# Optimization experiments

Hardware: AMD Instinct MI355X
Metric: run time of the kernel (lower is better)

The kernel has to match this reference:

```python
import jax, jax.numpy as jnp
import numpy as np

GAMMA = 20.0
GAMMA2 = 10.0
KATZ_FACTOR = 0.5
EPS = 1e-8


def setup_inputs() -> dict:
    key = jax.random.key(0)
    k1, k2, k3, k4 = jax.random.split(key, 4)
    b, n_way, k_shot, q, c, h, w = 16, 5, 5, 75, 640, 5, 5
    return {
        "support_xf": jax.random.normal(k1, (b, n_way * k_shot, c, h, w), jnp.float32),
        "support_y": jax.random.randint(k2, (b, n_way * k_shot), 0, n_way),
        "query_xf": jax.random.normal(k3, (b, q, c, h, w), jnp.float32),
        "query_y": jax.random.randint(k4, (b, q), 0, n_way),
        "n_way": n_way,
        "k_shot": k_shot,
    }


def _mel_loss(support_xf, query_xf, query_y, n_way, k_shot):
    b, s, c, h, w = support_xf.shape
    q = query_xf.shape[1]
    hw = h * w
    # averaging-based similarities: mean over shots, cosine over channel dim
    sup = support_xf.reshape(b, n_way, k_shot, c, hw).mean(2)          # (b, n_way, c, hw)
    sup = sup / (jnp.linalg.norm(sup, axis=2, keepdims=True) + EPS)
    qry = query_xf.reshape(b, q, c, hw)                                 # (b, q, c, hw)
    qry = qry / (jnp.linalg.norm(qry, axis=2, keepdims=True) + EPS)
    # S[b,q,way,i,j] = cos(query pixel i, support pixel j)
    S = jnp.einsum('bqci,bwcj->bqwij', qry, sup)                        # (b, q, n_way, hw, hw)
    M_q = hw
    M_s = n_way * hw
    S = S.transpose(0, 1, 3, 2, 4).reshape(b * q, M_q, M_s)             # (N, M_q, M_s)
    N = b * q

    # gamma-scaled softmax transition matrices
    T_sq = jax.nn.softmax(GAMMA * S, axis=-1)                           # (N, M_q, M_s)
    T_qs = jax.nn.softmax(GAMMA2 * jnp.swapaxes(S, -1, -2), axis=-1)    # (N, M_s, M_q)

    # bipartite block transition matrix T (N, M_s+M_q, M_s+M_q)
    top = jnp.concatenate([jnp.zeros((N, M_s, M_s), S.dtype),
                           jnp.swapaxes(T_sq, -1, -2)], axis=-1)
    bot = jnp.concatenate([jnp.swapaxes(T_qs, -1, -2),
                           jnp.zeros((N, M_q, M_q), S.dtype)], axis=-1)
    T = jnp.concatenate([top, bot], axis=-2)

    # katz = (inv(I - a*T) - I) @ 1  ==  solve(I - a*T, 1) - 1
    A = jnp.eye(M_s + M_q, dtype=S.dtype) - KATZ_FACTOR * T
    ones = jnp.ones((N, M_s + M_q, 1), S.dtype)
    katz = jnp.linalg.solve(A, ones)[..., 0] - 1.0                      # (N, M_s+M_q)

    pk = katz[:, :M_s]
    pk = pk / pk.sum(-1, keepdims=True)
    predicts = pk.reshape(N, n_way, -1).sum(-1)                         # (N, n_way)

    yv = query_y.reshape(N)
    logp = jnp.log(predicts)
    loss = -jnp.mean(logp[jnp.arange(N), yv])                           # NLLLoss
    return loss


def reference(support_xf, support_y, query_xf, query_y, n_way, k_shot):
    return _mel_loss(support_xf, query_xf, query_y, n_way, k_shot)
```

## Files before the change

### kernel.cpp

```cpp
#include <hip/hip_runtime.h>
#include <math.h>

#define NN   1200
#define EPSF 1e-8f

typedef _Float16 h8 __attribute__((ext_vector_type(8)));
typedef __attribute__((ext_vector_type(16))) float f16v;

#define AHI 0
#define ALO 16384
#define BHI 32768
#define BLO 49152

__global__ __launch_bounds__(256) void kA1(const float* __restrict__ sxf,
                                           float* __restrict__ supmean) {
  const int blk = blockIdx.x;
  const int b = blk / 25, rem = blk % 25, w = rem / 5, ck = rem % 5;
  const int c0 = ck * 128;
  const int tid = threadIdx.x;
  __shared__ float lds[3200];
  const float* base = sxf + (size_t)(b * 25 + w * 5) * 16000 + (size_t)c0 * 25;

  for (int f0 = tid * 4; f0 < 3200; f0 += 1024) {
    float4 a  = *(const float4*)(base + f0);
    float4 b1 = *(const float4*)(base + 16000 + f0);
    float4 c1 = *(const float4*)(base + 32000 + f0);
    float4 d1 = *(const float4*)(base + 48000 + f0);
    float4 e1 = *(const float4*)(base + 64000 + f0);
    lds[f0 + 0] = (a.x + b1.x + c1.x + d1.x + e1.x) * 0.2f;
    lds[f0 + 1] = (a.y + b1.y + c1.y + d1.y + e1.y) * 0.2f;
    lds[f0 + 2] = (a.z + b1.z + c1.z + d1.z + e1.z) * 0.2f;
    lds[f0 + 3] = (a.w + b1.w + c1.w + d1.w + e1.w) * 0.2f;
  }
  __syncthreads();
  for (int g = tid; g < 3200; g += 256) {
    int j = g >> 7, cc = g & 127;
    supmean[(size_t)(b * 125 + w * 25 + j) * 640 + c0 + cc] = lds[cc * 25 + j];
  }
}

__global__ __launch_bounds__(256) void kA2(const float* __restrict__ supmean,
                                           ushort* __restrict__ sup) {
  const int r = blockIdx.x * 4 + (threadIdx.x >> 6);
  const int lane = threadIdx.x & 63;
  const int b = r / 125, s = r % 125;
  const float* row = supmean + (size_t)r * 640;
  float4 v0 = *(const float4*)(row + lane * 4);
  float4 v1 = *(const float4*)(row + 256 + lane * 4);
  float4 v2 = {0.f, 0.f, 0.f, 0.f};
  if (lane < 32) v2 = *(const float4*)(row + 512 + lane * 4);
  float ssq = v0.x*v0.x + v0.y*v0.y + v0.z*v0.z + v0.w*v0.w
            + v1.x*v1.x + v1.y*v1.y + v1.z*v1.z + v1.w*v1.w
            + v2.x*v2.x + v2.y*v2.y + v2.z*v2.z + v2.w*v2.w;
#pragma unroll
  for (int d = 32; d; d >>= 1) ssq += __shfl_xor(ssq, d);
  const float rinv = 1.f / (sqrtf(ssq) + EPSF);
  ushort* dst = sup + (size_t)b * 160000 + (size_t)s * 640;
#pragma unroll
  for (int seg = 0; seg < 3; ++seg) {
    if (seg == 2 && lane >= 32) break;
    float4 v = (seg == 0) ? v0 : ((seg == 1) ? v1 : v2);
    int c = seg * 256 + lane * 4;
    float vv[4] = { v.x * rinv, v.y * rinv, v.z * rinv, v.w * rinv };
    ushort hh[4], ll[4];
#pragma unroll
    for (int u = 0; u < 4; ++u) {
      _Float16 h = (_Float16)vv[u];
      float rr = vv[u] - (float)h;
      _Float16 l = (_Float16)rr;
      hh[u] = __builtin_bit_cast(ushort, h);
      ll[u] = __builtin_bit_cast(ushort, l);
    }
    uint2 ph = { (uint)hh[0] | ((uint)hh[1] << 16), (uint)hh[2] | ((uint)hh[3] << 16) };
    uint2 pl = { (uint)ll[0] | ((uint)ll[1] << 16), (uint)ll[2] | ((uint)ll[3] << 16) };
    *(uint2*)(dst + c) = ph;
    *(uint2*)(dst + 80000 + c) = pl;
  }
}

__device__ __forceinline__ void load_chunk(const float* __restrict__ qbase5,
                                           const ushort* __restrict__ supb,
                                           int k0, int tid,
                                           float (&aq)[8][4], uint4 (&bq)[8]) {
#pragma unroll
  for (int j = 0; j < 8; ++j) {
    int t = tid + j * 256;
    if (t < 2000) {
      int q = t / 400, rem = t % 400, c4 = rem / 25, i = rem % 25;
      const float* qp = qbase5 + (size_t)q * 16000 + (size_t)(k0 + c4 * 4) * 25 + i;
      aq[j][0] = qp[0]; aq[j][1] = qp[25]; aq[j][2] = qp[50]; aq[j][3] = qp[75];
    }
  }
#pragma unroll
  for (int j = 0; j < 8; ++j) {
    int t = tid + j * 256;
    if (t < 2000) {
      int hl = (t >= 1000) ? 1 : 0;
      int r2 = t - hl * 1000;
      int row = r2 >> 3, seg = r2 & 7;
      bq[j] = *(const uint4*)(supb + (size_t)hl * 80000 + (size_t)row * 640 + k0 + seg * 8);
    }
  }
}

__device__ __forceinline__ void store_chunk(char* st, int tid,
                                            float (&aq)[8][4], uint4 (&bq)[8],
                                            float (&pn)[8]) {
#pragma unroll
  for (int j = 0; j < 8; ++j) {
    int t = tid + j * 256;
    if (t < 2000) {
      int q = t / 400, rem = t % 400, c4 = rem / 25, i = rem % 25;
      int row = q * 25 + i;
      ushort hh[4], ll[4];
      float ss = 0.f;
#pragma unroll
      for (int u = 0; u < 4; ++u) {
        float v = aq[j][u];
        ss = fmaf(v, v, ss);
        _Float16 h = (_Float16)v;
        float rr = v - (float)h;
        _Float16 l = (_Float16)rr;
        hh[u] = __builtin_bit_cast(ushort, h);
        ll[u] = __builtin_bit_cast(ushort, l);
      }
      pn[j] += ss;
      uint2 ph = { (uint)hh[0] | ((uint)hh[1] << 16), (uint)hh[2] | ((uint)hh[3] << 16) };
      uint2 pl = { (uint)ll[0] | ((uint)ll[1] << 16), (uint)ll[2] | ((uint)ll[3] << 16) };
      int off = (row * 128 + c4 * 8) ^ ((row & 7) << 4);
      *(uint2*)(st + AHI + off) = ph;
      *(uint2*)(st + ALO + off) = pl;
    }
  }
#pragma unroll
  for (int j = 0; j < 8; ++j) {
    int t = tid + j * 256;
    if (t < 2000) {
      int hl = (t >= 1000) ? 1 : 0;
      int r2 = t - hl * 1000;
      int row = r2 >> 3, seg = r2 & 7;
      int off = (row * 128 + seg * 16) ^ ((row & 7) << 4);
      *(uint4*)(st + BHI + hl * 16384 + off) = bq[j];
    }
  }
}

__global__ __launch_bounds__(256, 1) void kG(const float* __restrict__ qxf,
                                             const ushort* __restrict__ sup,
                                             float* __restrict__ Sg) {
  const int blk = blockIdx.x;
  const int b = blk / 15, qg = blk % 15;
  const int tid = threadIdx.x;
  const int lane = tid & 63, l31 = lane & 31, hi32 = lane >> 5;
  const int wv = tid >> 6, wr = wv >> 1, wc = wv & 1;
  __shared__ __align__(16) char st[65536];
  __shared__ float nsq[128], rinv_s[128];

  const float* qbase5 = qxf + (size_t)(b * 75 + qg * 5) * 16000;
  const ushort* supb = sup + (size_t)b * 160000;

  if (tid < 96) {
    int r = 125 + tid / 32, cb = (tid % 32) * 4;
    int off = (r * 128 + cb) ^ ((r & 7) << 4);
    *(uint*)(st + AHI + off) = 0u; *(uint*)(st + ALO + off) = 0u;
    *(uint*)(st + BHI + off) = 0u; *(uint*)(st + BLO + off) = 0u;
  }
  if (tid < 128) nsq[tid] = 0.f;

  f16v acc[2][2];
#pragma unroll
  for (int rt = 0; rt < 2; ++rt)
#pragma unroll
    for (int ct = 0; ct < 2; ++ct)
#pragma unroll
      for (int r = 0; r < 16; ++r) acc[rt][ct][r] = 0.f;

  float aA[8][4], aB[8][4];
  uint4 bA[8], bB[8];
  float pn[8];
#pragma unroll
  for (int j = 0; j < 8; ++j) pn[j] = 0.f;

  load_chunk(qbase5, supb, 0, tid, aA, bA);

#define MFMA_PHASE()                                                          \
  {                                                                           \
    _Pragma("unroll")                                                         \
    for (int ks = 0; ks < 4; ++ks) {                                          \
      const int kb = ks * 32 + hi32 * 16;                                     \
      h8 ahf[2], alf[2], bhf[2], blf[2];                                      \
      _Pragma("unroll")                                                       \
      for (int rt = 0; rt < 2; ++rt) {                                        \
        int ar = wr * 64 + rt * 32 + l31;                                     \
        int off = (ar * 128 + kb) ^ ((ar & 7) << 4);                          \
        ahf[rt] = *(const h8*)(st + AHI + off);                               \
        alf[rt] = *(const h8*)(st + ALO + off);                               \
      }                                                                       \
      _Pragma("unroll")                                                       \
      for (int ct = 0; ct < 2; ++ct) {                                        \
        int br = wc * 64 + ct * 32 + l31;                                     \
        int off = (br * 128 + kb) ^ ((br & 7) << 4);                          \
        bhf[ct] = *(const h8*)(st + BHI + off);                               \
        blf[ct] = *(const h8*)(st + BLO + off);                               \
      }                                                                       \
      _Pragma("unroll")                                                       \
      for (int rt = 0; rt < 2; ++rt)                                          \
        _Pragma("unroll")                                                     \
        for (int ct = 0; ct < 2; ++ct) {                                      \
          acc[rt][ct] = __builtin_amdgcn_mfma_f32_32x32x16_f16(ahf[rt], bhf[ct], acc[rt][ct], 0, 0, 0); \
          acc[rt][ct] = __builtin_amdgcn_mfma_f32_32x32x16_f16(alf[rt], bhf[ct], acc[rt][ct], 0, 0, 0); \
          acc[rt][ct] = __builtin_amdgcn_mfma_f32_32x32x16_f16(ahf[rt], blf[ct], acc[rt][ct], 0, 0, 0); \
        }                                                                     \
    }                                                                         \
  }

  for (int ch = 0; ch < 10; ch += 2) {
    __syncthreads();
    store_chunk(st, tid, aA, bA, pn);
    if (ch + 1 < 10) load_chunk(qbase5, supb, (ch + 1) * 64, tid, aB, bB);
    __syncthreads();
    MFMA_PHASE();
    __syncthreads();
    store_chunk(st, tid, aB, bB, pn);
    if (ch + 2 < 10) load_chunk(qbase5, supb, (ch + 2) * 64, tid, aA, bA);
    __syncthreads();
    MFMA_PHASE();
  }

#pragma unroll
  for (int j = 0; j < 8; ++j) {
    int t = tid + j * 256;
    if (t < 2000) {
      int q = t / 400, rem = t % 400, i = rem % 25;
      atomicAdd(&nsq[q * 25 + i], pn[j]);
    }
  }
  __syncthreads();
  if (tid < 125) rinv_s[tid] = 1.f / (sqrtf(nsq[tid]) + EPSF);
  __syncthreads();

#pragma unroll
  for (int rt = 0; rt < 2; ++rt) {
#pragma unroll
    for (int r = 0; r < 16; ++r) {
      int rowg = wr * 64 + rt * 32 + (r & 3) + 8 * (r >> 2) + 4 * hi32;
      if (rowg < 125) {
        float rv = rinv_s[rowg];
        int n = b * 75 + qg * 5 + rowg / 25;
        int i = rowg % 25;
#pragma unroll
        for (int ct = 0; ct < 2; ++ct) {
          int col = wc * 64 + ct * 32 + l31;
          Sg[(size_t)n * 3200 + i * 128 + col] = acc[rt][ct][r] * rv;
        }
      }
    }
  }
}

#define LD 132
__global__ __launch_bounds__(256) void kT(const float* __restrict__ Sg,
                                          const int* __restrict__ qy,
                                          float* __restrict__ out) {
  const int n = blockIdx.x;
  const int tid = threadIdx.x;
  __shared__ __align__(16) float S[25 * LD];
  __shared__ __align__(16) float TqsT[25 * LD];
  __shared__ float Bm[625], rhs[25], xv[25], Pk[5];

  const float* sgn = Sg + (size_t)n * 3200;
  for (int idx = tid; idx < 800; idx += 256) {
    int row = idx >> 5, q4 = idx & 31;
    *(float4*)(S + row * LD + q4 * 4) = *(const float4*)(sgn + row * 128 + q4 * 4);
  }
  if (tid < 5) Pk[tid] = 0.f;
  if (tid >= 32 && tid < 57) {
    int i = tid - 32;
    TqsT[i * LD + 125] = 0.f; TqsT[i * LD + 126] = 0.f; TqsT[i * LD + 127] = 0.f;
  }
  __syncthreads();

  if (tid < 125) {
    float mx = -1e30f;
#pragma unroll
    for (int i = 0; i < 25; ++i) mx = fmaxf(mx, S[i * LD + tid]);
    float sm = 0.f;
#pragma unroll
    for (int i = 0; i < 25; ++i) {
      float e = __expf(10.f * (S[i * LD + tid] - mx));
      TqsT[i * LD + tid] = e; sm += e;
    }
    float rs = 1.f / sm;
#pragma unroll
    for (int i = 0; i < 25; ++i) TqsT[i * LD + tid] *= rs;
  }
  __syncthreads();
  if (tid < 200) {
    int i = tid >> 3, l = tid & 7;
    float* Srow = S + i * LD;
    float mx = -1e30f;
    for (int ss = l; ss < 125; ss += 8) mx = fmaxf(mx, Srow[ss]);
    mx = fmaxf(mx, __shfl_xor(mx, 1, 8));
    mx = fmaxf(mx, __shfl_xor(mx, 2, 8));
    mx = fmaxf(mx, __shfl_xor(mx, 4, 8));
    float sm = 0.f;
    for (int ss = l; ss < 128; ss += 8) {
      float e = 0.f;
      if (ss < 125) { e = __expf(20.f * (Srow[ss] - mx)); sm += e; }
      Srow[ss] = e;
    }
    sm += __shfl_xor(sm, 1, 8);
    sm += __shfl_xor(sm, 2, 8);
    sm += __shfl_xor(sm, 4, 8);
    float rs = 1.f / sm;
    for (int ss = l; ss < 125; ss += 8) Srow[ss] *= rs;
  }
  __syncthreads();

  for (int ii = tid; ii < 625; ii += 256) {
    int i = ii / 25, ip = ii % 25;
    const float* ta = TqsT + i * LD;
    const float* tb = S + ip * LD;
    float4 s4 = { 0.f, 0.f, 0.f, 0.f };
#pragma unroll
    for (int q4 = 0; q4 < 32; ++q4) {
      float4 a4 = *(const float4*)(ta + q4 * 4);
      float4 b4 = *(const float4*)(tb + q4 * 4);
      s4.x = fmaf(a4.x, b4.x, s4.x); s4.y = fmaf(a4.y, b4.y, s4.y);
      s4.z = fmaf(a4.z, b4.z, s4.z); s4.w = fmaf(a4.w, b4.w, s4.w);
    }
    Bm[ii] = (s4.x + s4.y) + (s4.z + s4.w);
  }
  if (tid < 25) {
    const float* ta = TqsT + tid * LD;
    float4 s4 = { 0.f, 0.f, 0.f, 0.f };
#pragma unroll
    for (int q4 = 0; q4 < 32; ++q4) {
      float4 a4 = *(const float4*)(ta + q4 * 4);
      s4.x += a4.x; s4.y += a4.y; s4.z += a4.z; s4.w += a4.w;
    }
    rhs[tid] = 1.f + 0.5f * ((s4.x + s4.y) + (s4.z + s4.w));
  }
  __syncthreads();

  if (tid < 64) {
    float Brow[25], x, rh;
    if (tid < 25) {
      rh = rhs[tid]; x = rh;
#pragma unroll
      for (int ip = 0; ip < 25; ++ip) Brow[ip] = Bm[tid * 25 + ip];
    } else {
      rh = 0.f; x = 0.f;
#pragma unroll
      for (int ip = 0; ip < 25; ++ip) Brow[ip] = 0.f;
    }
#pragma unroll
    for (int it = 0; it < 16; ++it) {
      float sum = 0.f;
#pragma unroll
      for (int ip = 0; ip < 25; ++ip) sum = fmaf(Brow[ip], __shfl(x, ip), sum);
      x = rh + 0.25f * sum;
    }
    if (tid < 25) xv[tid] = x;
  }
  __syncthreads();

  if (tid < 125) {
    float kz = 0.f;
#pragma unroll
    for (int i = 0; i < 25; ++i) kz = fmaf(S[i * LD + tid], xv[i], kz);
    atomicAdd(&Pk[tid / 25], kz);
  }
  __syncthreads();
  if (tid == 0) {
    float den = Pk[0] + Pk[1] + Pk[2] + Pk[3] + Pk[4];
    int y = qy[n];
    float v = -(logf(Pk[y]) - logf(den)) * (1.0f / (float)NN);
    atomicAdd(out, v);
  }
}

extern "C" void kernel_launch(void* const* d_in, const int* in_sizes, int n_in,
                              void* d_out, int out_size, void* d_ws, size_t ws_size,
                              hipStream_t stream) {
  const float* sxf = (const float*)d_in[0];
  const float* qxf = (const float*)d_in[2];
  const int*   qy  = (const int*)d_in[3];
  float* out = (float*)d_out;
  float*  supmean = (float*)d_ws;
  ushort* sup     = (ushort*)((char*)d_ws + 5120000);
  float*  Sgw     = (float*)((char*)d_ws + 10240000);

  hipMemsetAsync(out, 0, sizeof(float), stream);
  kA1<<<400, 256, 0, stream>>>(sxf, supmean);
  kA2<<<500, 256, 0, stream>>>(supmean, sup);
  kG<<<240, 256, 0, stream>>>(qxf, sup, Sgw);
  kT<<<NN, 256, 0, stream>>>(Sgw, qy, out);
}
```

Baseline: 257.3 us.

## Fuse Katz solve into GEMM kernel and pre-swizzle support for direct LDS loads

Merges the per-query softmax/Katz kernel into the similarity GEMM kernel, so each block processes its 5 queries from LDS instead of writing S to global memory and relaunching. The support tensor is now stored pre-chunked and pre-swizzled, so it can be copied straight into LDS with global_load_lds. The register double-buffered prefetch is replaced with a single-buffer load-then-compute loop. This removes the S round trip and one launch, but the post-processing now runs on only 240 blocks sequentially over 5 queries rather than 1200 blocks, and loads no longer overlap with compute.

```diff
diff --git a/kernel.cpp b/kernel.cpp
--- a/kernel.cpp
+++ b/kernel.cpp
@@ -40,7 +40,7 @@
 }
 
 __global__ __launch_bounds__(256) void kA2(const float* __restrict__ supmean,
-                                           ushort* __restrict__ sup) {
+                                           char* __restrict__ sup) {
   const int r = blockIdx.x * 4 + (threadIdx.x >> 6);
   const int lane = threadIdx.x & 63;
   const int b = r / 125, s = r % 125;
@@ -55,117 +55,56 @@
 #pragma unroll
   for (int d = 32; d; d >>= 1) ssq += __shfl_xor(ssq, d);
   const float rinv = 1.f / (sqrtf(ssq) + EPSF);
-  ushort* dst = sup + (size_t)b * 160000 + (size_t)s * 640;
+  char* base = sup + (size_t)b * 320000;
 #pragma unroll
   for (int seg = 0; seg < 3; ++seg) {
     if (seg == 2 && lane >= 32) break;
     float4 v = (seg == 0) ? v0 : ((seg == 1) ? v1 : v2);
     int c = seg * 256 + lane * 4;
+    int ch = c >> 6, c64 = c & 63;
+    int off = s * 128 + (((c64 >> 3) << 4) ^ ((s & 7) << 4)) + (c64 & 7) * 2;
     float vv[4] = { v.x * rinv, v.y * rinv, v.z * rinv, v.w * rinv };
     ushort hh[4], ll[4];
 #pragma unroll
     for (int u = 0; u < 4; ++u) {
       _Float16 h = (_Float16)vv[u];
-      float rr = vv[u] - (float)h;
-      _Float16 l = (_Float16)rr;
+      _Float16 l = (_Float16)(vv[u] - (float)h);
       hh[u] = __builtin_bit_cast(ushort, h);
       ll[u] = __builtin_bit_cast(ushort, l);
     }
     uint2 ph = { (uint)hh[0] | ((uint)hh[1] << 16), (uint)hh[2] | ((uint)hh[3] << 16) };
     uint2 pl = { (uint)ll[0] | ((uint)ll[1] << 16), (uint)ll[2] | ((uint)ll[3] << 16) };
-    *(uint2*)(dst + c) = ph;
-    *(uint2*)(dst + 80000 + c) = pl;
+    *(uint2*)(base + ch * 32000 + off) = ph;
+    *(uint2*)(base + ch * 32000 + 16000 + off) = pl;
   }
 }
 
-__device__ __forceinline__ void load_chunk(const float* __restrict__ qbase5,
-                                           const ushort* __restrict__ supb,
-                                           int k0, int tid,
-                                           float (&aq)[8][4], uint4 (&bq)[8]) {
-#pragma unroll
-  for (int j = 0; j < 8; ++j) {
-    int t = tid + j * 256;
-    if (t < 2000) {
-      int q = t / 400, rem = t % 400, c4 = rem / 25, i = rem % 25;
-      const float* qp = qbase5 + (size_t)q * 16000 + (size_t)(k0 + c4 * 4) * 25 + i;
-      aq[j][0] = qp[0]; aq[j][1] = qp[25]; aq[j][2] = qp[50]; aq[j][3] = qp[75];
-    }
-  }
-#pragma unroll
-  for (int j = 0; j < 8; ++j) {
-    int t = tid + j * 256;
-    if (t < 2000) {
-      int hl = (t >= 1000) ? 1 : 0;
-      int r2 = t - hl * 1000;
-      int row = r2 >> 3, seg = r2 & 7;
-      bq[j] = *(const uint4*)(supb + (size_t)hl * 80000 + (size_t)row * 640 + k0 + seg * 8);
-    }
-  }
-}
-
-__device__ __forceinline__ void store_chunk(char* st, int tid,
-                                            float (&aq)[8][4], uint4 (&bq)[8],
-                                            float (&pn)[8]) {
-#pragma unroll
-  for (int j = 0; j < 8; ++j) {
-    int t = tid + j * 256;
-    if (t < 2000) {
-      int q = t / 400, rem = t % 400, c4 = rem / 25, i = rem % 25;
-      int row = q * 25 + i;
-      ushort hh[4], ll[4];
-      float ss = 0.f;
-#pragma unroll
-      for (int u = 0; u < 4; ++u) {
-        float v = aq[j][u];
-        ss = fmaf(v, v, ss);
-        _Float16 h = (_Float16)v;
-        float rr = v - (float)h;
-        _Float16 l = (_Float16)rr;
-        hh[u] = __builtin_bit_cast(ushort, h);
-        ll[u] = __builtin_bit_cast(ushort, l);
-      }
-      pn[j] += ss;
-      uint2 ph = { (uint)hh[0] | ((uint)hh[1] << 16), (uint)hh[2] | ((uint)hh[3] << 16) };
-      uint2 pl = { (uint)ll[0] | ((uint)ll[1] << 16), (uint)ll[2] | ((uint)ll[3] << 16) };
-      int off = (row * 128 + c4 * 8) ^ ((row & 7) << 4);
-      *(uint2*)(st + AHI + off) = ph;
-      *(uint2*)(st + ALO + off) = pl;
-    }
-  }
-#pragma unroll
-  for (int j = 0; j < 8; ++j) {
-    int t = tid + j * 256;
-    if (t < 2000) {
-      int hl = (t >= 1000) ? 1 : 0;
-      int r2 = t - hl * 1000;
-      int row = r2 >> 3, seg = r2 & 7;
-      int off = (row * 128 + seg * 16) ^ ((row & 7) << 4);
-      *(uint4*)(st + BHI + hl * 16384 + off) = bq[j];
-    }
-  }
-}
-
 __global__ __launch_bounds__(256, 1) void kG(const float* __restrict__ qxf,
-                                             const ushort* __restrict__ sup,
-                                             float* __restrict__ Sg) {
+                                             const int* __restrict__ qy,
+                                             const char* __restrict__ sup,
+                                             float* __restrict__ out) {
   const int blk = blockIdx.x;
   const int b = blk / 15, qg = blk % 15;
   const int tid = threadIdx.x;
   const int lane = tid & 63, l31 = lane & 31, hi32 = lane >> 5;
   const int wv = tid >> 6, wr = wv >> 1, wc = wv & 1;
   __shared__ __align__(16) char st[65536];
-  __shared__ float nsq[128], rinv_s[128];
+  __shared__ __align__(16) float TqsT[25 * 128];
+  __shared__ float Bm[625];
+  __shared__ float nsq[125], rinv_s[125], rhs[25], xv[25], Pk[5];
 
   const float* qbase5 = qxf + (size_t)(b * 75 + qg * 5) * 16000;
-  const ushort* supb = sup + (size_t)b * 160000;
+  const char*  supb   = sup + (size_t)b * 320000;
 
   if (tid < 96) {
-    int r = 125 + tid / 32, cb = (tid % 32) * 4;
-    int off = (r * 128 + cb) ^ ((r & 7) << 4);
-    *(uint*)(st + AHI + off) = 0u; *(uint*)(st + ALO + off) = 0u;
-    *(uint*)(st + BHI + off) = 0u; *(uint*)(st + BLO + off) = 0u;
-  }
-  if (tid < 128) nsq[tid] = 0.f;
+    uint4 z = {0u, 0u, 0u, 0u};
+    *(uint4*)(st + (tid / 24) * 16384 + 16000 + (tid % 24) * 16) = z;
+  }
+  if (tid < 125) nsq[tid] = 0.f;
+  if (tid >= 128 && tid < 203) {
+    int k = tid - 128;
+    TqsT[(k / 3) * 128 + 125 + (k % 3)] = 0.f;
+  }
 
   f16v acc[2][2];
 #pragma unroll
@@ -175,63 +114,86 @@
 #pragma unroll
       for (int r = 0; r < 16; ++r) acc[rt][ct][r] = 0.f;
 
-  float aA[8][4], aB[8][4];
-  uint4 bA[8], bB[8];
   float pn[8];
 #pragma unroll
   for (int j = 0; j < 8; ++j) pn[j] = 0.f;
 
-  load_chunk(qbase5, supb, 0, tid, aA, bA);
-
-#define MFMA_PHASE()                                                          \
-  {                                                                           \
-    _Pragma("unroll")                                                         \
-    for (int ks = 0; ks < 4; ++ks) {                                          \
-      const int kb = ks * 32 + hi32 * 16;                                     \
-      h8 ahf[2], alf[2], bhf[2], blf[2];                                      \
-      _Pragma("unroll")                                                       \
-      for (int rt = 0; rt < 2; ++rt) {                                        \
-        int ar = wr * 64 + rt * 32 + l31;                                     \
-        int off = (ar * 128 + kb) ^ ((ar & 7) << 4);                          \
-        ahf[rt] = *(const h8*)(st + AHI + off);                               \
-        alf[rt] = *(const h8*)(st + ALO + off);                               \
-      }                                                                       \
-      _Pragma("unroll")                                                       \
-      for (int ct = 0; ct < 2; ++ct) {                                        \
-        int br = wc * 64 + ct * 32 + l31;                                     \
-        int off = (br * 128 + kb) ^ ((br & 7) << 4);                          \
-        bhf[ct] = *(const h8*)(st + BHI + off);                               \
-        blf[ct] = *(const h8*)(st + BLO + off);                               \
-      }                                                                       \
-      _Pragma("unroll")                                                       \
-      for (int rt = 0; rt < 2; ++rt)                                          \
-        _Pragma("unroll")                                                     \
-        for (int ct = 0; ct < 2; ++ct) {                                      \
-          acc[rt][ct] = __builtin_amdgcn_mfma_f32_32x32x16_f16(ahf[rt], bhf[ct], acc[rt][ct], 0, 0, 0); \
-          acc[rt][ct] = __builtin_amdgcn_mfma_f32_32x32x16_f16(alf[rt], bhf[ct], acc[rt][ct], 0, 0, 0); \
-          acc[rt][ct] = __builtin_amdgcn_mfma_f32_32x32x16_f16(ahf[rt], blf[ct], acc[rt][ct], 0, 0, 0); \
-        }                                                                     \
-    }                                                                         \
-  }
-
-  for (int ch = 0; ch < 10; ch += 2) {
-    __syncthreads();
-    store_chunk(st, tid, aA, bA, pn);
-    if (ch + 1 < 10) load_chunk(qbase5, supb, (ch + 1) * 64, tid, aB, bB);
-    __syncthreads();
-    MFMA_PHASE();
-    __syncthreads();
-    store_chunk(st, tid, aB, bB, pn);
-    if (ch + 2 < 10) load_chunk(qbase5, supb, (ch + 2) * 64, tid, aA, bA);
-    __syncthreads();
-    MFMA_PHASE();
+  for (int ch = 0; ch < 10; ++ch) {
+    const int k0 = ch * 64;
+#pragma unroll
+    for (int j = 0; j < 4; ++j) {
+      int t = tid + j * 256;
+      if (t < 1000) {
+        const char* gh = supb + ch * 32000 + t * 16;
+        __builtin_amdgcn_global_load_lds(
+            (const __attribute__((address_space(1))) uint*)gh,
+            (__attribute__((address_space(3))) uint*)(st + BHI + t * 16), 16, 0, 0);
+        __builtin_amdgcn_global_load_lds(
+            (const __attribute__((address_space(1))) uint*)(gh + 16000),
+            (__attribute__((address_space(3))) uint*)(st + BLO + t * 16), 16, 0, 0);
+      }
+    }
+#pragma unroll
+    for (int j = 0; j < 8; ++j) {
+      int t = tid + j * 256;
+      if (t < 2000) {
+        int q = t / 400, rem = t % 400, c4 = rem / 25, i = rem % 25;
+        const float* qp = qbase5 + (size_t)q * 16000 + (size_t)(k0 + c4 * 4) * 25 + i;
+        float w0 = qp[0], w1 = qp[25], w2 = qp[50], w3 = qp[75];
+        pn[j] = fmaf(w0, w0, fmaf(w1, w1, fmaf(w2, w2, fmaf(w3, w3, pn[j]))));
+        float vv[4] = { w0, w1, w2, w3 };
+        ushort hh[4], ll[4];
+#pragma unroll
+        for (int u = 0; u < 4; ++u) {
+          _Float16 h = (_Float16)vv[u];
+          _Float16 l = (_Float16)(vv[u] - (float)h);
+          hh[u] = __builtin_bit_cast(ushort, h);
+          ll[u] = __builtin_bit_cast(ushort, l);
+        }
+        uint2 ph = { (uint)hh[0] | ((uint)hh[1] << 16), (uint)hh[2] | ((uint)hh[3] << 16) };
+        uint2 pl = { (uint)ll[0] | ((uint)ll[1] << 16), (uint)ll[2] | ((uint)ll[3] << 16) };
+        int r = q * 25 + i, c64 = c4 * 4;
+        int off = r * 128 + (((c64 >> 3) << 4) ^ ((r & 7) << 4)) + (c64 & 7) * 2;
+        *(uint2*)(st + AHI + off) = ph;
+        *(uint2*)(st + ALO + off) = pl;
+      }
+    }
+    __syncthreads();
+#pragma unroll
+    for (int ks = 0; ks < 4; ++ks) {
+      const int kb = ks * 32 + hi32 * 16;
+      h8 ahf[2], alf[2], bhf[2], blf[2];
+#pragma unroll
+      for (int rt = 0; rt < 2; ++rt) {
+        int ar = wr * 64 + rt * 32 + l31;
+        int off = ar * 128 + (kb ^ ((ar & 7) << 4));
+        ahf[rt] = *(const h8*)(st + AHI + off);
+        alf[rt] = *(const h8*)(st + ALO + off);
+      }
+#pragma unroll
+      for (int ct = 0; ct < 2; ++ct) {
+        int br = wc * 64 + ct * 32 + l31;
+        int off = br * 128 + (kb ^ ((br & 7) << 4));
+        bhf[ct] = *(const h8*)(st + BHI + off);
+        blf[ct] = *(const h8*)(st + BLO + off);
+      }
+#pragma unroll
+      for (int rt = 0; rt < 2; ++rt)
+#pragma unroll
+        for (int ct = 0; ct < 2; ++ct) {
+          acc[rt][ct] = __builtin_amdgcn_mfma_f32_32x32x16_f16(ahf[rt], bhf[ct], acc[rt][ct], 0, 0, 0);
+          acc[rt][ct] = __builtin_amdgcn_mfma_f32_32x32x16_f16(alf[rt], bhf[ct], acc[rt][ct], 0, 0, 0);
+          acc[rt][ct] = __builtin_amdgcn_mfma_f32_32x32x16_f16(ahf[rt], blf[ct], acc[rt][ct], 0, 0, 0);
+        }
+    }
+    __syncthreads();
   }
 
 #pragma unroll
   for (int j = 0; j < 8; ++j) {
     int t = tid + j * 256;
     if (t < 2000) {
-      int q = t / 400, rem = t % 400, i = rem % 25;
+      int q = t / 400, i = (t % 400) % 25;
       atomicAdd(&nsq[q * 25 + i], pn[j]);
     }
   }
@@ -239,6 +201,7 @@
   if (tid < 125) rinv_s[tid] = 1.f / (sqrtf(nsq[tid]) + EPSF);
   __syncthreads();
 
+  float* S = (float*)st;
 #pragma unroll
   for (int rt = 0; rt < 2; ++rt) {
 #pragma unroll
@@ -246,138 +209,115 @@
       int rowg = wr * 64 + rt * 32 + (r & 3) + 8 * (r >> 2) + 4 * hi32;
       if (rowg < 125) {
         float rv = rinv_s[rowg];
-        int n = b * 75 + qg * 5 + rowg / 25;
-        int i = rowg % 25;
 #pragma unroll
         for (int ct = 0; ct < 2; ++ct) {
           int col = wc * 64 + ct * 32 + l31;
-          Sg[(size_t)n * 3200 + i * 128 + col] = acc[rt][ct][r] * rv;
+          S[rowg * 128 + col] = acc[rt][ct][r] * rv;
         }
       }
     }
   }
-}
-
-#define LD 132
-__global__ __launch_bounds__(256) void kT(const float* __restrict__ Sg,
-                                          const int* __restrict__ qy,
-                                          float* __restrict__ out) {
-  const int n = blockIdx.x;
-  const int tid = threadIdx.x;
-  __shared__ __align__(16) float S[25 * LD];
-  __shared__ __align__(16) float TqsT[25 * LD];
-  __shared__ float Bm[625], rhs[25], xv[25], Pk[5];
-
-  const float* sgn = Sg + (size_t)n * 3200;
-  for (int idx = tid; idx < 800; idx += 256) {
-    int row = idx >> 5, q4 = idx & 31;
-    *(float4*)(S + row * LD + q4 * 4) = *(const float4*)(sgn + row * 128 + q4 * 4);
-  }
-  if (tid < 5) Pk[tid] = 0.f;
-  if (tid >= 32 && tid < 57) {
-    int i = tid - 32;
-    TqsT[i * LD + 125] = 0.f; TqsT[i * LD + 126] = 0.f; TqsT[i * LD + 127] = 0.f;
-  }
   __syncthreads();
 
-  if (tid < 125) {
-    float mx = -1e30f;
-#pragma unroll
-    for (int i = 0; i < 25; ++i) mx = fmaxf(mx, S[i * LD + tid]);
-    float sm = 0.f;
-#pragma unroll
-    for (int i = 0; i < 25; ++i) {
-      float e = __expf(10.f * (S[i * LD + tid] - mx));
-      TqsT[i * LD + tid] = e; sm += e;
-    }
-    float rs = 1.f / sm;
-#pragma unroll
-    for (int i = 0; i < 25; ++i) TqsT[i * LD + tid] *= rs;
-  }
-  __syncthreads();
-  if (tid < 200) {
-    int i = tid >> 3, l = tid & 7;
-    float* Srow = S + i * LD;
-    float mx = -1e30f;
-    for (int ss = l; ss < 125; ss += 8) mx = fmaxf(mx, Srow[ss]);
-    mx = fmaxf(mx, __shfl_xor(mx, 1, 8));
-    mx = fmaxf(mx, __shfl_xor(mx, 2, 8));
-    mx = fmaxf(mx, __shfl_xor(mx, 4, 8));
-    float sm = 0.f;
-    for (int ss = l; ss < 128; ss += 8) {
-      float e = 0.f;
-      if (ss < 125) { e = __expf(20.f * (Srow[ss] - mx)); sm += e; }
-      Srow[ss] = e;
-    }
-    sm += __shfl_xor(sm, 1, 8);
-    sm += __shfl_xor(sm, 2, 8);
-    sm += __shfl_xor(sm, 4, 8);
-    float rs = 1.f / sm;
-    for (int ss = l; ss < 125; ss += 8) Srow[ss] *= rs;
-  }
-  __syncthreads();
-
-  for (int ii = tid; ii < 625; ii += 256) {
-    int i = ii / 25, ip = ii % 25;
-    const float* ta = TqsT + i * LD;
-    const float* tb = S + ip * LD;
-    float4 s4 = { 0.f, 0.f, 0.f, 0.f };
-#pragma unroll
-    for (int q4 = 0; q4 < 32; ++q4) {
-      float4 a4 = *(const float4*)(ta + q4 * 4);
-      float4 b4 = *(const float4*)(tb + q4 * 4);
-      s4.x = fmaf(a4.x, b4.x, s4.x); s4.y = fmaf(a4.y, b4.y, s4.y);
-      s4.z = fmaf(a4.z, b4.z, s4.z); s4.w = fmaf(a4.w, b4.w, s4.w);
-    }
-    Bm[ii] = (s4.x + s4.y) + (s4.z + s4.w);
-  }
-  if (tid < 25) {
-    const float* ta = TqsT + tid * LD;
-    float4 s4 = { 0.f, 0.f, 0.f, 0.f };
-#pragma unroll
-    for (int q4 = 0; q4 < 32; ++q4) {
-      float4 a4 = *(const float4*)(ta + q4 * 4);
-      s4.x += a4.x; s4.y += a4.y; s4.z += a4.z; s4.w += a4.w;
-    }
-    rhs[tid] = 1.f + 0.5f * ((s4.x + s4.y) + (s4.z + s4.w));
-  }
-  __syncthreads();
-
-  if (tid < 64) {
-    float Brow[25], x, rh;
+  float lsum = 0.f;
+  for (int q5 = 0; q5 < 5; ++q5) {
+    float* Sq = S + q5 * 25 * 128;
+    if (tid < 125) {
+      float mx = -1e30f;
+#pragma unroll
+      for (int i = 0; i < 25; ++i) mx = fmaxf(mx, Sq[i * 128 + tid]);
+      float sm = 0.f;
+      float ev[25];
+#pragma unroll
+      for (int i = 0; i < 25; ++i) { ev[i] = __expf(10.f * (Sq[i * 128 + tid] - mx)); sm += ev[i]; }
+      float rs = 1.f / sm;
+#pragma unroll
+      for (int i = 0; i < 25; ++i) TqsT[i * 128 + tid] = ev[i] * rs;
+    }
+    if (tid >= 200 && tid < 205) Pk[tid - 200] = 0.f;
+    __syncthreads();
+    if (tid < 200) {
+      int i = tid >> 3, l = tid & 7;
+      float* Srow = Sq + i * 128;
+      float mx = -1e30f;
+      for (int ss = l; ss < 125; ss += 8) mx = fmaxf(mx, Srow[ss]);
+      mx = fmaxf(mx, __shfl_xor(mx, 1, 8));
+      mx = fmaxf(mx, __shfl_xor(mx, 2, 8));
+      mx = fmaxf(mx, __shfl_xor(mx, 4, 8));
+      float sm = 0.f;
+      for (int ss = l; ss < 128; ss += 8) {
+        float e = 0.f;
+        if (ss < 125) { e = __expf(20.f * (Srow[ss] - mx)); sm += e; }
+        Srow[ss] = e;
+      }
+      sm += __shfl_xor(sm, 1, 8);
+      sm += __shfl_xor(sm, 2, 8);
+      sm += __shfl_xor(sm, 4, 8);
+      float rs = 1.f / sm;
+      for (int ss = l; ss < 125; ss += 8) Srow[ss] *= rs;
+    }
+    __syncthreads();
+    for (int ii = tid; ii < 625; ii += 256) {
+      int i = ii / 25, ip = ii % 25;
+      const float* ta = TqsT + i * 128;
+      const float* tb = Sq + ip * 128;
+      float4 s4 = { 0.f, 0.f, 0.f, 0.f };
+#pragma unroll
+      for (int q4 = 0; q4 < 32; ++q4) {
+        float4 a4 = *(const float4*)(ta + q4 * 4);
+        float4 b4 = *(const float4*)(tb + q4 * 4);
+        s4.x = fmaf(a4.x, b4.x, s4.x); s4.y = fmaf(a4.y, b4.y, s4.y);
+        s4.z = fmaf(a4.z, b4.z, s4.z); s4.w = fmaf(a4.w, b4.w, s4.w);
+      }
+      Bm[ii] = (s4.x + s4.y) + (s4.z + s4.w);
+    }
     if (tid < 25) {
-      rh = rhs[tid]; x = rh;
-#pragma unroll
-      for (int ip = 0; ip < 25; ++ip) Brow[ip] = Bm[tid * 25 + ip];
-    } else {
-      rh = 0.f; x = 0.f;
-#pragma unroll
-      for (int ip = 0; ip < 25; ++ip) Brow[ip] = 0.f;
-    }
-#pragma unroll
-    for (int it = 0; it < 16; ++it) {
-      float sum = 0.f;
-#pragma unroll
-      for (int ip = 0; ip < 25; ++ip) sum = fmaf(Brow[ip], __shfl(x, ip), sum);
-      x = rh + 0.25f * sum;
-    }
-    if (tid < 25) xv[tid] = x;
-  }
-  __syncthreads();
-
-  if (tid < 125) {
-    float kz = 0.f;
-#pragma unroll
-    for (int i = 0; i < 25; ++i) kz = fmaf(S[i * LD + tid], xv[i], kz);
-    atomicAdd(&Pk[tid / 25], kz);
-  }
-  __syncthreads();
-  if (tid == 0) {
-    float den = Pk[0] + Pk[1] + Pk[2] + Pk[3] + Pk[4];
-    int y = qy[n];
-    float v = -(logf(Pk[y]) - logf(den)) * (1.0f / (float)NN);
-    atomicAdd(out, v);
-  }
+      const float* ta = TqsT + tid * 128;
+      float4 s4 = { 0.f, 0.f, 0.f, 0.f };
+#pragma unroll
+      for (int q4 = 0; q4 < 32; ++q4) {
+        float4 a4 = *(const float4*)(ta + q4 * 4);
+        s4.x += a4.x; s4.y += a4.y; s4.z += a4.z; s4.w += a4.w;
+      }
+      rhs[tid] = 1.f + 0.5f * ((s4.x + s4.y) + (s4.z + s4.w));
+    }
+    __syncthreads();
+    if (tid < 64) {
+      float Brow[25], x, rh;
+      if (tid < 25) {
+        rh = rhs[tid]; x = rh;
+#pragma unroll
+        for (int ip = 0; ip < 25; ++ip) Brow[ip] = Bm[tid * 25 + ip];
+      } else {
+        rh = 0.f; x = 0.f;
+#pragma unroll
+        for (int ip = 0; ip < 25; ++ip) Brow[ip] = 0.f;
+      }
+#pragma unroll
+      for (int it = 0; it < 16; ++it) {
+        float sum = 0.f;
+#pragma unroll
+        for (int ip = 0; ip < 25; ++ip) sum = fmaf(Brow[ip], __shfl(x, ip), sum);
+        x = rh + 0.25f * sum;
+      }
+      if (tid < 25) xv[tid] = x;
+    }
+    __syncthreads();
+    if (tid < 125) {
+      float kz = 0.f;
+#pragma unroll
+      for (int i = 0; i < 25; ++i) kz = fmaf(Sq[i * 128 + tid], xv[i], kz);
+      atomicAdd(&Pk[tid / 25], kz);
+    }
+    __syncthreads();
+    if (tid == 0) {
+      float den = Pk[0] + Pk[1] + Pk[2] + Pk[3] + Pk[4];
+      int y = qy[b * 75 + qg * 5 + q5];
+      lsum += logf(den) - logf(Pk[y]);
+    }
+    __syncthreads();
+  }
+  if (tid == 0) atomicAdd(out, lsum * (1.0f / (float)NN));
 }
 
 extern "C" void kernel_launch(void* const* d_in, const int* in_sizes, int n_in,
@@ -387,13 +327,11 @@
   const float* qxf = (const float*)d_in[2];
   const int*   qy  = (const int*)d_in[3];
   float* out = (float*)d_out;
-  float*  supmean = (float*)d_ws;
-  ushort* sup     = (ushort*)((char*)d_ws + 5120000);
-  float*  Sgw     = (float*)((char*)d_ws + 10240000);
+  float* supmean = (float*)d_ws;
+  char*  sup     = (char*)d_ws + 5120000;
 
   hipMemsetAsync(out, 0, sizeof(float), stream);
   kA1<<<400, 256, 0, stream>>>(sxf, supmean);
   kA2<<<500, 256, 0, stream>>>(supmean, sup);
-  kG<<<240, 256, 0, stream>>>(qxf, sup, Sgw);
-  kT<<<NN, 256, 0, stream>>>(Sgw, qy, out);
+  kG<<<240, 256, 0, stream>>>(qxf, qy, sup, out);
 }
```

New measurement: 271.6 us. 1.06x slower.
